# Optimization experiments

Measured on AMD Instinct MI355X. Metric: run time of the kernel, lower is better.

## Reference

```python
import jax, jax.numpy as jnp
import numpy as np

N_NODES = 50000
N_EDGES = 1600000
N_GRAPHS = 64


def setup_inputs() -> dict:
    key = jax.random.key(0)
    ks = jax.random.split(key, 16)
    p = lambda k, shape: (jax.random.normal(k, shape, dtype=jnp.float32) * 0.05)
    x = jax.random.normal(ks[0], (N_NODES, 128), dtype=jnp.float32)
    edge_index = jax.random.randint(ks[1], (2, N_EDGES), 0, N_NODES, dtype=jnp.int32)
    edge_attr = jax.random.uniform(ks[2], (N_EDGES,), dtype=jnp.float32)
    batch = jnp.sort(jax.random.randint(ks[3], (N_NODES,), 0, N_GRAPHS, dtype=jnp.int32))
    return {
        'x': x, 'edge_index': edge_index, 'edge_attr': edge_attr, 'batch': batch,
        'W1': p(ks[4], (128, 128)), 'b1': jnp.zeros((128,), jnp.float32),
        'W2': p(ks[5], (128, 64)), 'b2': jnp.zeros((64,), jnp.float32),
        'gW1': p(ks[6], (64, 32)), 'gb1': jnp.zeros((32,), jnp.float32),
        'gW2': p(ks[7], (32, 1)), 'gb2': jnp.zeros((1,), jnp.float32),
        'fcW1': p(ks[8], (64, 128)), 'fcb1': jnp.zeros((128,), jnp.float32),
        'fcW2': p(ks[9], (128, 2)), 'fcb2': jnp.zeros((2,), jnp.float32),
    }


def gcn_conv(x, src, dst, ew, W, b):
    # PyG GCNConv with edge weights: add self-loops (weight 1), symmetric norm.
    xw = x @ W  # [N, out]
    deg = jax.ops.segment_sum(ew, dst, num_segments=N_NODES) + 1.0  # self-loop
    dinv = jnp.where(deg > 0, jax.lax.rsqrt(deg), 0.0)
    coef = dinv[src] * ew * dinv[dst]  # [E]
    agg = jax.ops.segment_sum(coef[:, None] * xw[src], dst, num_segments=N_NODES)
    agg = agg + (dinv * dinv)[:, None] * xw  # self-loop contribution
    return agg + b


def global_attention(x, batch, gW1, gb1, gW2, gb2):
    # gate_nn: Linear(64,32)->ReLU->Linear(32,1), segment-softmax over graphs
    g = (jax.nn.relu(x @ gW1 + gb1) @ gW2 + gb2)[:, 0]  # [N]
    gmax = jax.ops.segment_max(g, batch, num_segments=N_GRAPHS)
    ex = jnp.exp(g - gmax[batch])
    den = jax.ops.segment_sum(ex, batch, num_segments=N_GRAPHS)
    alpha = ex / den[batch]
    return jax.ops.segment_sum(alpha[:, None] * x, batch, num_segments=N_GRAPHS)


def reference(x, edge_index, edge_attr, batch, W1, b1, W2, b2,
              gW1, gb1, gW2, gb2, fcW1, fcb1, fcW2, fcb2):
    src, dst = edge_index[0], edge_index[1]
    h = jax.nn.relu(gcn_conv(x, src, dst, edge_attr, W1, b1))
    x1 = jax.nn.relu(gcn_conv(h, src, dst, edge_attr, W2, b2))
    x2 = global_attention(x1, batch, gW1, gb1, gW2, gb2)  # [G, 64]
    # dropout is identity in eval mode
    h2 = jax.nn.relu(x2 @ fcW1 + fcb1)
    logits = h2 @ fcW2 + fcb2
    return jax.nn.log_softmax(logits, axis=1)
```

## Files before the change

### kernel.cpp

```cpp
#include <hip/hip_runtime.h>
#include <hip/hip_bf16.h>
#include <hip/hip_fp16.h>

#define N_NODES 50000
#define N_EDGES 1600000
#define N_GRAPHS 64
#define G1BLKS 1563
#define NSH 8
#define SH_STRIDE 50048
#define NBLK8 6250

__device__ __forceinline__ float coef_of(unsigned p) {
    return __half2float(__ushort_as_half((unsigned short)(p & 0xFFFFu)));
}

__global__ void mega1(const float* __restrict__ X, const float* __restrict__ W,
                      __half* __restrict__ Yh, const int* __restrict__ dst,
                      const float* __restrict__ ew,
                      unsigned long long* __restrict__ packed8,
                      unsigned short* __restrict__ pos16) {
    __shared__ float Xl[32][132];
    if (blockIdx.x >= G1BLKS) {
        const int sh = blockIdx.x & (NSH - 1);
        unsigned long long* __restrict__ pk = packed8 + (size_t)sh * SH_STRIDE;
        int e = (blockIdx.x - G1BLKS) * 256 + threadIdx.x;
        if (e < N_EDGES) {
            int d = __builtin_nontemporal_load(&dst[e]);
            float w = __builtin_nontemporal_load(&ew[e]);
            unsigned fix = (unsigned)(w * 16777216.0f);
            unsigned long long old = atomicAdd(&pk[d], 0x100000000ull | (unsigned long long)fix);
            pos16[e] = (unsigned short)((sh << 12) | (unsigned)(old >> 32));
        }
        return;
    }
    const int rt = threadIdx.x >> 5;
    const int ct = threadIdx.x & 31;
    const int base = blockIdx.x * 32;
    for (int i = threadIdx.x; i < 32 * 32; i += 256) {
        int rr = i >> 5, cc = (i & 31) << 2;
        int gr = base + rr;
        float4 v = (gr < N_NODES) ? *(const float4*)&X[(size_t)gr * 128 + cc]
                                  : make_float4(0.f, 0.f, 0.f, 0.f);
        Xl[rr][cc] = v.x; Xl[rr][cc + 1] = v.y; Xl[rr][cc + 2] = v.z; Xl[rr][cc + 3] = v.w;
    }
    __syncthreads();
    float acc[4][4] = {};
    for (int k = 0; k < 128; k += 4) {
        float4 a0 = *(const float4*)&Xl[rt * 4 + 0][k];
        float4 a1 = *(const float4*)&Xl[rt * 4 + 1][k];
        float4 a2 = *(const float4*)&Xl[rt * 4 + 2][k];
        float4 a3 = *(const float4*)&Xl[rt * 4 + 3][k];
        float4 w0 = *(const float4*)&W[(size_t)(k + 0) * 128 + ct * 4];
        float4 w1 = *(const float4*)&W[(size_t)(k + 1) * 128 + ct * 4];
        float4 w2 = *(const float4*)&W[(size_t)(k + 2) * 128 + ct * 4];
        float4 w3 = *(const float4*)&W[(size_t)(k + 3) * 128 + ct * 4];
        #define STEP(av, wv)  \
            acc[0][0] += av##0 * wv.x; acc[0][1] += av##0 * wv.y; acc[0][2] += av##0 * wv.z; acc[0][3] += av##0 * wv.w; \
            acc[1][0] += av##1 * wv.x; acc[1][1] += av##1 * wv.y; acc[1][2] += av##1 * wv.z; acc[1][3] += av##1 * wv.w; \
            acc[2][0] += av##2 * wv.x; acc[2][1] += av##2 * wv.y; acc[2][2] += av##2 * wv.z; acc[2][3] += av##2 * wv.w; \
            acc[3][0] += av##3 * wv.x; acc[3][1] += av##3 * wv.y; acc[3][2] += av##3 * wv.z; acc[3][3] += av##3 * wv.w;
        { float ax0=a0.x, ax1=a1.x, ax2=a2.x, ax3=a3.x; STEP(ax, w0) }
        { float ay0=a0.y, ay1=a1.y, ay2=a2.y, ay3=a3.y; STEP(ay, w1) }
        { float az0=a0.z, az1=a1.z, az2=a2.z, az3=a3.z; STEP(az, w2) }
        { float aw0=a0.w, aw1=a1.w, aw2=a2.w, aw3=a3.w; STEP(aw, w3) }
        #undef STEP
    }
    const int pc = ct >> 3;
    const int cw = (ct & 7) * 4;
    for (int i = 0; i < 4; ++i) {
        int gr = base + rt * 4 + i;
        if (gr < N_NODES) {
            ushort4 u;
            u.x = __half_as_ushort(__float2half(acc[i][0]));
            u.y = __half_as_ushort(__float2half(acc[i][1]));
            u.z = __half_as_ushort(__float2half(acc[i][2]));
            u.w = __half_as_ushort(__float2half(acc[i][3]));
            *(ushort4*)&Yh[((size_t)pc * N_NODES + gr) * 32 + cw] = u;
        }
    }
}

__global__ void block_sums_dinv(const unsigned long long* __restrict__ packed8,
                                int* __restrict__ bsum, float* __restrict__ dinv) {
    __shared__ int s[256];
    int idx = blockIdx.x * 256 + threadIdx.x;
    int c = 0;
    if (idx < N_NODES) {
        unsigned long long csum = 0, fsum = 0;
        #pragma unroll
        for (int sh = 0; sh < NSH; ++sh) {
            unsigned long long p = packed8[(size_t)sh * SH_STRIDE + idx];
            csum += p >> 32;
            fsum += p & 0xFFFFFFFFull;
        }
        c = (int)csum;
        dinv[idx] = rsqrtf((float)fsum * (1.0f / 16777216.0f) + 1.0f);
    }
    s[threadIdx.x] = c;
    __syncthreads();
    for (int o = 128; o; o >>= 1) {
        if (threadIdx.x < o) s[threadIdx.x] += s[threadIdx.x + o];
        __syncthreads();
    }
    if (threadIdx.x == 0) bsum[blockIdx.x] = s[0];
}

__global__ void scan_bsums(const int* __restrict__ bsum, int* __restrict__ boff,
                           int nb, int* __restrict__ row_start_last) {
    __shared__ int s[256];
    int v = (threadIdx.x < nb) ? bsum[threadIdx.x] : 0;
    s[threadIdx.x] = v;
    __syncthreads();
    for (int o = 1; o < 256; o <<= 1) {
        int t = 0;
        if (threadIdx.x >= o) t = s[threadIdx.x - o];
        __syncthreads();
        s[threadIdx.x] += t;
        __syncthreads();
    }
    if (threadIdx.x < nb) boff[threadIdx.x] = s[threadIdx.x] - v;
    if (threadIdx.x == 0) *row_start_last = N_EDGES;
}

__global__ void scan_counts(const unsigned long long* __restrict__ packed8,
                            const int* __restrict__ boff, int* __restrict__ row_start,
                            int* __restrict__ soff) {
    __shared__ int s[256];
    int idx = blockIdx.x * 256 + threadIdx.x;
    int cs[NSH];
    int v = 0;
    if (idx < N_NODES) {
        #pragma unroll
        for (int sh = 0; sh < NSH; ++sh) {
            cs[sh] = (int)(packed8[(size_t)sh * SH_STRIDE + idx] >> 32);
            v += cs[sh];
        }
    }
    s[threadIdx.x] = v;
    __syncthreads();
    for (int o = 1; o < 256; o <<= 1) {
        int t = 0;
        if (threadIdx.x >= o) t = s[threadIdx.x - o];
        __syncthreads();
        s[threadIdx.x] += t;
        __syncthreads();
    }
    if (idx < N_NODES) {
        int ex = boff[blockIdx.x] + s[threadIdx.x] - v;
        row_start[idx] = ex;
        int run = ex;
        #pragma unroll
        for (int sh = 0; sh < NSH; ++sh) {
            soff[(size_t)sh * SH_STRIDE + idx] = run;
            run += cs[sh];
        }
    }
}

__global__ void fill_direct(const int* __restrict__ src, const int* __restrict__ dst,
                            const float* __restrict__ ew, const unsigned short* __restrict__ pos16,
                            const int* __restrict__ soff, const float* __restrict__ dinv,
                            unsigned* __restrict__ csr) {
    int e = blockIdx.x * 256 + threadIdx.x;
    if (e < N_EDGES) {
        int d = __builtin_nontemporal_load(&dst[e]);
        int s = __builtin_nontemporal_load(&src[e]);
        float w = __builtin_nontemporal_load(&ew[e]);
        unsigned p16 = (unsigned)__builtin_nontemporal_load(&pos16[e]);
        int sh = (int)(p16 >> 12);
        int p  = (int)(p16 & 0xFFFu);
        float coef = dinv[s] * w * dinv[d];
        csr[soff[(size_t)sh * SH_STRIDE + d] + p] = ((unsigned)s << 16) | __half_as_ushort(__float2half(coef));
    }
}

template<int NP, bool HOUT>
__global__ void agg_csr_pair(const int* __restrict__ row_start, const unsigned* __restrict__ csr,
                             const __half* __restrict__ xwh, const float* __restrict__ dinv,
                             const float* __restrict__ b, void* __restrict__ outp) {
    constexpr int OUT = NP * 32;
    const int c    = blockIdx.x / NBLK8;
    const int nb   = blockIdx.x % NBLK8;
    const int n    = nb * 8 + (threadIdx.x >> 5);
    const int kk   = threadIdx.x & 15;
    const int half = (threadIdx.x >> 4) & 1;
    if (n >= N_NODES) return;
    const __half* __restrict__ bp = xwh + ((size_t)c * N_NODES) * 32 + 2 * kk;
    const int beg = row_start[n], end = row_start[n + 1];
    float ax = 0.f, ay = 0.f;
    int i = beg + half;
    unsigned c0 = 0, c1 = 0, c2 = 0, c3 = 0;
    if (i + 6 < end) { c0 = csr[i]; c1 = csr[i + 2]; c2 = csr[i + 4]; c3 = csr[i + 6]; }
    while (i + 6 < end) {
        __half2 h0 = *(const __half2*)(bp + (size_t)(c0 >> 16) * 32);
        __half2 h1 = *(const __half2*)(bp + (size_t)(c1 >> 16) * 32);
        __half2 h2 = *(const __half2*)(bp + (size_t)(c2 >> 16) * 32);
        __half2 h3 = *(const __half2*)(bp + (size_t)(c3 >> 16) * 32);
        float e0 = coef_of(c0), e1 = coef_of(c1), e2 = coef_of(c2), e3 = coef_of(c3);
        int ni = i + 8;
        unsigned d0 = 0, d1 = 0, d2 = 0, d3 = 0;
        if (ni + 6 < end) { d0 = csr[ni]; d1 = csr[ni + 2]; d2 = csr[ni + 4]; d3 = csr[ni + 6]; }
        float2 f0 = __half22float2(h0), f1 = __half22float2(h1);
        float2 f2 = __half22float2(h2), f3 = __half22float2(h3);
        ax += e0 * f0.x + e1 * f1.x + e2 * f2.x + e3 * f3.x;
        ay += e0 * f0.y + e1 * f1.y + e2 * f2.y + e3 * f3.y;
        c0 = d0; c1 = d1; c2 = d2; c3 = d3;
        i = ni;
    }
    for (; i < end; i += 2) {
        unsigned p = csr[i];
        float2 f = __half22float2(*(const __half2*)(bp + (size_t)(p >> 16) * 32));
        float e = coef_of(p);
        ax += e * f.x; ay += e * f.y;
    }
    ax += __shfl_xor(ax, 16);
    ay += __shfl_xor(ay, 16);
    if (half == 0) {
        float2 sf = __half22float2(*(const __half2*)(bp + (size_t)n * 32));
        float dv = dinv[n];
        float dv2 = dv * dv;
        int kg = c * 32 + 2 * kk;
        float ox = fmaxf(ax + dv2 * sf.x + b[kg], 0.f);
        float oy = fmaxf(ay + dv2 * sf.y + b[kg + 1], 0.f);
        if constexpr (HOUT) {
            __half* o = (__half*)outp;
            *(__half2*)&o[(size_t)n * OUT + kg] = __floats2half2_rn(ox, oy);
        } else {
            float* o = (float*)outp;
            *(float2*)&o[(size_t)n * OUT + kg] = make_float2(ox, oy);
        }
    }
}

__global__ void gemm2_reg(const __half* __restrict__ Xh, const float* __restrict__ W,
                          __half* __restrict__ Yh, int nrows) {
    __shared__ float Xl[32][132];
    __shared__ float Wl[128][64];
    const int rt = threadIdx.x >> 5;
    const int ct = threadIdx.x & 31;
    const int base = blockIdx.x * 32;
    for (int i = threadIdx.x; i < 32 * 32; i += 256) {
        int rr = i >> 5, cc = (i & 31) << 2;
        int gr = base + rr;
        float2 fa = make_float2(0.f, 0.f), fb = fa;
        if (gr < nrows) {
            const __half2* ph = (const __half2*)&Xh[(size_t)gr * 128 + cc];
            fa = __half22float2(ph[0]);
            fb = __half22float2(ph[1]);
        }
        Xl[rr][cc] = fa.x; Xl[rr][cc + 1] = fa.y; Xl[rr][cc + 2] = fb.x; Xl[rr][cc + 3] = fb.y;
    }
    for (int i = threadIdx.x; i < 128 * 16; i += 256) {
        int kk = i >> 4, cc = (i & 15) << 2;
        *(float4*)&Wl[kk][cc] = *(const float4*)&W[(size_t)kk * 64 + cc];
    }
    float acc[4][2] = {};
    __syncthreads();
    for (int k = 0; k < 128; k += 4) {
        float4 a0 = *(const float4*)&Xl[rt * 4 + 0][k];
        float4 a1 = *(const float4*)&Xl[rt * 4 + 1][k];
        float4 a2 = *(const float4*)&Xl[rt * 4 + 2][k];
        float4 a3 = *(const float4*)&Xl[rt * 4 + 3][k];
        float2 w0 = *(const float2*)&Wl[k + 0][ct * 2];
        float2 w1 = *(const float2*)&Wl[k + 1][ct * 2];
        float2 w2 = *(const float2*)&Wl[k + 2][ct * 2];
        float2 w3 = *(const float2*)&Wl[k + 3][ct * 2];
        acc[0][0] += a0.x * w0.x; acc[0][1] += a0.x * w0.y;
        acc[1][0] += a1.x * w0.x; acc[1][1] += a1.x * w0.y;
        acc[2][0] += a2.x * w0.x; acc[2][1] += a2.x * w0.y;
        acc[3][0] += a3.x * w0.x; acc[3][1] += a3.x * w0.y;
        acc[0][0] += a0.y * w1.x; acc[0][1] += a0.y * w1.y;
        acc[1][0] += a1.y * w1.x; acc[1][1] += a1.y * w1.y;
        acc[2][0] += a2.y * w1.x; acc[2][1] += a2.y * w1.y;
        acc[3][0] += a3.y * w1.x; acc[3][1] += a3.y * w1.y;
        acc[0][0] += a0.z * w2.x; acc[0][1] += a0.z * w2.y;
        acc[1][0] += a1.z * w2.x; acc[1][1] += a1.z * w2.y;
        acc[2][0] += a2.z * w2.x; acc[2][1] += a2.z * w2.y;
        acc[3][0] += a3.z * w2.x; acc[3][1] += a3.z * w2.y;
        acc[0][0] += a0.w * w3.x; acc[0][1] += a0.w * w3.y;
        acc[1][0] += a1.w * w3.x; acc[1][1] += a1.w * w3.y;
        acc[2][0] += a2.w * w3.x; acc[2][1] += a2.w * w3.y;
        acc[3][0] += a3.w * w3.x; acc[3][1] += a3.w * w3.y;
    }
    const int col0 = ct * 2;
    const int pc   = col0 >> 5;
    const int cw   = col0 & 31;
    for (int i = 0; i < 4; ++i) {
        int gr = base + rt * 4 + i;
        if (gr < nrows) {
            __half2 hv = __floats2half2_rn(acc[i][0], acc[i][1]);
            *(__half2*)&Yh[((size_t)pc * nrows + gr) * 32 + cw] = hv;
        }
    }
}

__global__ void gate_pool(const __half* __restrict__ x1h, const float* __restrict__ gW1,
                          const float* __restrict__ gb1, const float* __restrict__ gW2,
                          const float* __restrict__ gb2, const int* __restrict__ batch,
                          float* __restrict__ den, float* __restrict__ pooledU) {
    __shared__ float W1l[64 * 32];
    __shared__ float W2l[32];
    __shared__ float b1l[32];
    __shared__ float Xs[256][65];
    __shared__ float el[256];
    for (int i = threadIdx.x; i < 64 * 32; i += 256) W1l[i] = gW1[i];
    if (threadIdx.x < 32) { W2l[threadIdx.x] = gW2[threadIdx.x]; b1l[threadIdx.x] = gb1[threadIdx.x]; }
    const int n0 = blockIdx.x * 256;
    for (int i = threadIdx.x; i < 256 * 16; i += 256) {
        int r = i >> 4, c4 = (i & 15) << 2;
        int nn = n0 + r;
        if (nn < N_NODES) {
            ushort4 u = *(const ushort4*)&x1h[(size_t)nn * 64 + c4];
            Xs[r][c4 + 0] = __half2float(__ushort_as_half(u.x));
            Xs[r][c4 + 1] = __half2float(__ushort_as_half(u.y));
            Xs[r][c4 + 2] = __half2float(__ushort_as_half(u.z));
            Xs[r][c4 + 3] = __half2float(__ushort_as_half(u.w));
        } else {
            Xs[r][c4 + 0] = 0.f; Xs[r][c4 + 1] = 0.f;
            Xs[r][c4 + 2] = 0.f; Xs[r][c4 + 3] = 0.f;
        }
    }
    __syncthreads();
    const float gb2v = gb2[0];
    const int n = n0 + threadIdx.x;
    float ev = 0.f;
    if (n < N_NODES) {
        float t[32];
        #pragma unroll
        for (int j = 0; j < 32; ++j) t[j] = b1l[j];
        for (int k = 0; k < 64; ++k) {
            float xv = Xs[threadIdx.x][k];
            #pragma unroll
            for (int j = 0; j < 32; ++j) t[j] += xv * W1l[k * 32 + j];
        }
        float a = gb2v;
        #pragma unroll
        for (int j = 0; j < 32; ++j) a += fmaxf(t[j], 0.f) * W2l[j];
        ev = expf(a);
    }
    el[threadIdx.x] = ev;
    __syncthreads();
    const int f   = threadIdx.x & 63;
    const int grp = threadIdx.x >> 6;
    int start = n0 + grp * 64;
    if (start >= N_NODES) return;
    int end = min(start + 64, N_NODES);
    int cur = batch[start];
    float acc = 0.f, accd = 0.f;
    for (int m = start; m < end; ++m) {
        int bb = batch[m];
        if (bb != cur) {
            atomicAdd(&pooledU[cur * 64 + f], acc);
            if (f == 0) atomicAdd(&den[cur], accd);
            acc = 0.f; accd = 0.f; cur = bb;
        }
        float e = el[m - n0];
        acc += e * Xs[m - n0][f];
        if (f == 0) accd += e;
    }
    atomicAdd(&pooledU[cur * 64 + f], acc);
    if (f == 0) atomicAdd(&den[cur], accd);
}

__global__ void head_kernel(const float* __restrict__ pooledU, const float* __restrict__ den,
                            const float* __restrict__ fcW1, const float* __restrict__ fcb1,
                            const float* __restrict__ fcW2, const float* __restrict__ fcb2,
                            float* __restrict__ out) {
    __shared__ float P[64];
    __shared__ float r0[2], r1[2];
    const int gi = blockIdx.x;
    if (threadIdx.x < 64) P[threadIdx.x] = pooledU[gi * 64 + threadIdx.x] / den[gi];
    __syncthreads();
    const int j = threadIdx.x;
    float a = fcb1[j];
    #pragma unroll 8
    for (int k = 0; k < 64; ++k) a += P[k] * fcW1[k * 128 + j];
    float h = fmaxf(a, 0.f);
    float p0 = h * fcW2[j * 2 + 0];
    float p1 = h * fcW2[j * 2 + 1];
    for (int o = 32; o; o >>= 1) { p0 += __shfl_xor(p0, o); p1 += __shfl_xor(p1, o); }
    if ((threadIdx.x & 63) == 0) { r0[threadIdx.x >> 6] = p0; r1[threadIdx.x >> 6] = p1; }
    __syncthreads();
    if (threadIdx.x == 0) {
        float l0 = r0[0] + r0[1] + fcb2[0];
        float l1 = r1[0] + r1[1] + fcb2[1];
        float m = fmaxf(l0, l1);
        float lse = m + logf(expf(l0 - m) + expf(l1 - m));
        out[gi * 2 + 0] = l0 - lse;
        out[gi * 2 + 1] = l1 - lse;
    }
}

extern "C" void kernel_launch(void* const* d_in, const int* in_sizes, int n_in,
                              void* d_out, int out_size, void* d_ws, size_t ws_size,
                              hipStream_t stream) {
    const float* x    = (const float*)d_in[0];
    const int*   ei   = (const int*)d_in[1];
    const float* ew   = (const float*)d_in[2];
    const int*   batch= (const int*)d_in[3];
    const float* W1   = (const float*)d_in[4];
    const float* b1   = (const float*)d_in[5];
    const float* W2   = (const float*)d_in[6];
    const float* b2   = (const float*)d_in[7];
    const float* gW1  = (const float*)d_in[8];
    const float* gb1  = (const float*)d_in[9];
    const float* gW2  = (const float*)d_in[10];
    const float* gb2  = (const float*)d_in[11];
    const float* fcW1 = (const float*)d_in[12];
    const float* fcb1 = (const float*)d_in[13];
    const float* fcW2 = (const float*)d_in[14];
    const float* fcb2 = (const float*)d_in[15];
    float* out = (float*)d_out;

    const int* src = ei;
    const int* dst = ei + N_EDGES;

    const int EB = (N_EDGES + 255) / 256;
    const int NB = (N_NODES + 255) / 256;

    float* ws = (float*)d_ws;
    __half* xwh  = (__half*)ws;
    __half* hbuf = (__half*)(ws + 3200000);
    __half* x1h  = (__half*)(ws + 6400000);
    size_t off = 9600000;
    unsigned* csr   = (unsigned*)(ws + off); off += 1600000;
    unsigned short* pos16 = (unsigned short*)(ws + off); off += 800000;
    int*   row_start= (int*)(ws + off);    off += 50176;
    unsigned long long* packed8 = (unsigned long long*)(ws + off); off += 2 * NSH * SH_STRIDE;
    int*   soff     = (int*)(ws + off);    off += NSH * SH_STRIDE;
    float* dinv     = ws + off;            off += 50176;
    int*   bsum     = (int*)(ws + off);    off += 256;
    int*   boff     = (int*)(ws + off);    off += 256;
    float* den      = ws + off;            off += 64;
    float* pooled   = ws + off;            off += 4096;

    hipMemsetAsync(packed8, 0, (size_t)NSH * SH_STRIDE * sizeof(unsigned long long), stream);
    hipMemsetAsync(den, 0, (64 + 4096) * sizeof(float), stream);

    mega1<<<G1BLKS + EB, 256, 0, stream>>>(x, W1, xwh, dst, ew, packed8, pos16);

    block_sums_dinv<<<NB, 256, 0, stream>>>(packed8, bsum, dinv);
    scan_bsums<<<1, 256, 0, stream>>>(bsum, boff, NB, row_start + N_NODES);
    scan_counts<<<NB, 256, 0, stream>>>(packed8, boff, row_start, soff);
    fill_direct<<<EB, 256, 0, stream>>>(src, dst, ew, pos16, soff, dinv, csr);

    agg_csr_pair<4, true><<<4 * NBLK8, 256, 0, stream>>>(row_start, csr, xwh, dinv, b1, hbuf);

    gemm2_reg<<<(N_NODES + 31) / 32, 256, 0, stream>>>(hbuf, W2, xwh, N_NODES);
    agg_csr_pair<2, true><<<2 * NBLK8, 256, 0, stream>>>(row_start, csr, xwh, dinv, b2, x1h);

    gate_pool<<<NB, 256, 0, stream>>>(x1h, gW1, gb1, gW2, gb2, batch, den, pooled);

    head_kernel<<<N_GRAPHS, 128, 0, stream>>>(pooled, den, fcW1, fcb1, fcW2, fcb2, out);
}
```

Baseline: 298.1 us.

## Fuse CSR build stages into one cooperative kernel; deepen aggregation prefetch

Replaces the four CSR-construction kernels (block sums/dinv, block-sum scan, count scan, fill) with one cooperative kernel that separates phases with grid-wide syncs and fills edges via a grid-stride loop. It also zeroes the pooling accumulators inside that kernel, removing a memset. Separately, the CSR aggregation loop is software-pipelined one stage deeper, issuing gathers for the next group while the current group is accumulated. This cuts launch overhead and inter-kernel gaps, but grid.sync costs and the 1024-block grid may leave fewer waves in flight during the fill phase.

```diff
diff --git a/kernel.cpp b/kernel.cpp
--- a/kernel.cpp
+++ b/kernel.cpp
@@ -1,6 +1,9 @@
 #include <hip/hip_runtime.h>
 #include <hip/hip_bf16.h>
 #include <hip/hip_fp16.h>
+#include <hip/hip_cooperative_groups.h>
+
+namespace cg = cooperative_groups;
 
 #define N_NODES 50000
 #define N_EDGES 1600000
@@ -9,6 +12,7 @@
 #define NSH 8
 #define SH_STRIDE 50048
 #define NBLK8 6250
+#define COOP_BLKS 1024
 
 __device__ __forceinline__ float coef_of(unsigned p) {
     return __half2float(__ushort_as_half((unsigned short)(p & 0xFFFFu)));
@@ -80,97 +84,101 @@
     }
 }
 
-__global__ void block_sums_dinv(const unsigned long long* __restrict__ packed8,
-                                int* __restrict__ bsum, float* __restrict__ dinv) {
+__global__ void csr_build_coop(const unsigned long long* __restrict__ packed8,
+                               const int* __restrict__ src, const int* __restrict__ dst,
+                               const float* __restrict__ ew,
+                               const unsigned short* __restrict__ pos16,
+                               int* __restrict__ bsum, int* __restrict__ boff,
+                               int* __restrict__ row_start, int* __restrict__ soff,
+                               float* __restrict__ dinv, unsigned* __restrict__ csr,
+                               float* __restrict__ den_pool) {
+    cg::grid_group grid = cg::this_grid();
     __shared__ int s[256];
-    int idx = blockIdx.x * 256 + threadIdx.x;
+    const int tid = blockIdx.x * 256 + threadIdx.x;
+
     int c = 0;
-    if (idx < N_NODES) {
+    if (tid < N_NODES) {
         unsigned long long csum = 0, fsum = 0;
         #pragma unroll
         for (int sh = 0; sh < NSH; ++sh) {
-            unsigned long long p = packed8[(size_t)sh * SH_STRIDE + idx];
+            unsigned long long p = packed8[(size_t)sh * SH_STRIDE + tid];
             csum += p >> 32;
             fsum += p & 0xFFFFFFFFull;
         }
         c = (int)csum;
-        dinv[idx] = rsqrtf((float)fsum * (1.0f / 16777216.0f) + 1.0f);
-    }
-    s[threadIdx.x] = c;
-    __syncthreads();
-    for (int o = 128; o; o >>= 1) {
-        if (threadIdx.x < o) s[threadIdx.x] += s[threadIdx.x + o];
+        dinv[tid] = rsqrtf((float)fsum * (1.0f / 16777216.0f) + 1.0f);
+    }
+    if (tid < 64 + 4096) den_pool[tid] = 0.f;
+    if (blockIdx.x < 196) {
+        s[threadIdx.x] = c;
         __syncthreads();
-    }
-    if (threadIdx.x == 0) bsum[blockIdx.x] = s[0];
-}
-
-__global__ void scan_bsums(const int* __restrict__ bsum, int* __restrict__ boff,
-                           int nb, int* __restrict__ row_start_last) {
-    __shared__ int s[256];
-    int v = (threadIdx.x < nb) ? bsum[threadIdx.x] : 0;
-    s[threadIdx.x] = v;
-    __syncthreads();
-    for (int o = 1; o < 256; o <<= 1) {
-        int t = 0;
-        if (threadIdx.x >= o) t = s[threadIdx.x - o];
+        for (int o = 128; o; o >>= 1) {
+            if (threadIdx.x < o) s[threadIdx.x] += s[threadIdx.x + o];
+            __syncthreads();
+        }
+        if (threadIdx.x == 0) bsum[blockIdx.x] = s[0];
+    }
+    grid.sync();
+
+    if (blockIdx.x == 0) {
+        int v = (threadIdx.x < 196) ? bsum[threadIdx.x] : 0;
+        s[threadIdx.x] = v;
         __syncthreads();
-        s[threadIdx.x] += t;
+        for (int o = 1; o < 256; o <<= 1) {
+            int t = 0;
+            if (threadIdx.x >= o) t = s[threadIdx.x - o];
+            __syncthreads();
+            s[threadIdx.x] += t;
+            __syncthreads();
+        }
+        if (threadIdx.x < 196) boff[threadIdx.x] = s[threadIdx.x] - v;
+        if (threadIdx.x == 0) row_start[N_NODES] = N_EDGES;
+    }
+    grid.sync();
+
+    if (blockIdx.x < 196) {
+        int idx = tid;
+        int cs[NSH];
+        int v = 0;
+        if (idx < N_NODES) {
+            #pragma unroll
+            for (int sh = 0; sh < NSH; ++sh) {
+                cs[sh] = (int)(packed8[(size_t)sh * SH_STRIDE + idx] >> 32);
+                v += cs[sh];
+            }
+        }
+        s[threadIdx.x] = v;
         __syncthreads();
-    }
-    if (threadIdx.x < nb) boff[threadIdx.x] = s[threadIdx.x] - v;
-    if (threadIdx.x == 0) *row_start_last = N_EDGES;
-}
-
-__global__ void scan_counts(const unsigned long long* __restrict__ packed8,
-                            const int* __restrict__ boff, int* __restrict__ row_start,
-                            int* __restrict__ soff) {
-    __shared__ int s[256];
-    int idx = blockIdx.x * 256 + threadIdx.x;
-    int cs[NSH];
-    int v = 0;
-    if (idx < N_NODES) {
-        #pragma unroll
-        for (int sh = 0; sh < NSH; ++sh) {
-            cs[sh] = (int)(packed8[(size_t)sh * SH_STRIDE + idx] >> 32);
-            v += cs[sh];
-        }
-    }
-    s[threadIdx.x] = v;
-    __syncthreads();
-    for (int o = 1; o < 256; o <<= 1) {
-        int t = 0;
-        if (threadIdx.x >= o) t = s[threadIdx.x - o];
-        __syncthreads();
-        s[threadIdx.x] += t;
-        __syncthreads();
-    }
-    if (idx < N_NODES) {
-        int ex = boff[blockIdx.x] + s[threadIdx.x] - v;
-        row_start[idx] = ex;
-        int run = ex;
-        #pragma unroll
-        for (int sh = 0; sh < NSH; ++sh) {
-            soff[(size_t)sh * SH_STRIDE + idx] = run;
-            run += cs[sh];
-        }
-    }
-}
-
-__global__ void fill_direct(const int* __restrict__ src, const int* __restrict__ dst,
-                            const float* __restrict__ ew, const unsigned short* __restrict__ pos16,
-                            const int* __restrict__ soff, const float* __restrict__ dinv,
-                            unsigned* __restrict__ csr) {
-    int e = blockIdx.x * 256 + threadIdx.x;
-    if (e < N_EDGES) {
+        for (int o = 1; o < 256; o <<= 1) {
+            int t = 0;
+            if (threadIdx.x >= o) t = s[threadIdx.x - o];
+            __syncthreads();
+            s[threadIdx.x] += t;
+            __syncthreads();
+        }
+        if (idx < N_NODES) {
+            int ex = boff[blockIdx.x] + s[threadIdx.x] - v;
+            row_start[idx] = ex;
+            int run = ex;
+            #pragma unroll
+            for (int sh = 0; sh < NSH; ++sh) {
+                soff[(size_t)sh * SH_STRIDE + idx] = run;
+                run += cs[sh];
+            }
+        }
+    }
+    grid.sync();
+
+    const int stride = gridDim.x * 256;
+    for (int e = tid; e < N_EDGES; e += stride) {
         int d = __builtin_nontemporal_load(&dst[e]);
-        int s = __builtin_nontemporal_load(&src[e]);
+        int sv = __builtin_nontemporal_load(&src[e]);
         float w = __builtin_nontemporal_load(&ew[e]);
         unsigned p16 = (unsigned)__builtin_nontemporal_load(&pos16[e]);
         int sh = (int)(p16 >> 12);
         int p  = (int)(p16 & 0xFFFu);
-        float coef = dinv[s] * w * dinv[d];
-        csr[soff[(size_t)sh * SH_STRIDE + d] + p] = ((unsigned)s << 16) | __half_as_ushort(__float2half(coef));
+        float coef = dinv[sv] * w * dinv[d];
+        csr[soff[(size_t)sh * SH_STRIDE + d] + p] = ((unsigned)sv << 16) | __half_as_ushort(__float2half(coef));
     }
 }
 
@@ -189,23 +197,36 @@
     const int beg = row_start[n], end = row_start[n + 1];
     float ax = 0.f, ay = 0.f;
     int i = beg + half;
-    unsigned c0 = 0, c1 = 0, c2 = 0, c3 = 0;
-    if (i + 6 < end) { c0 = csr[i]; c1 = csr[i + 2]; c2 = csr[i + 4]; c3 = csr[i + 6]; }
+    unsigned ca0 = 0, ca1 = 0, ca2 = 0, ca3 = 0;
+    unsigned cb0 = 0, cb1 = 0, cb2 = 0, cb3 = 0;
+    __half2 ha0{}, ha1{}, ha2{}, ha3{};
+    if (i + 6 < end) {
+        ca0 = csr[i]; ca1 = csr[i + 2]; ca2 = csr[i + 4]; ca3 = csr[i + 6];
+        ha0 = *(const __half2*)(bp + (size_t)(ca0 >> 16) * 32);
+        ha1 = *(const __half2*)(bp + (size_t)(ca1 >> 16) * 32);
+        ha2 = *(const __half2*)(bp + (size_t)(ca2 >> 16) * 32);
+        ha3 = *(const __half2*)(bp + (size_t)(ca3 >> 16) * 32);
+        int i2 = i + 8;
+        if (i2 + 6 < end) { cb0 = csr[i2]; cb1 = csr[i2 + 2]; cb2 = csr[i2 + 4]; cb3 = csr[i2 + 6]; }
+    }
     while (i + 6 < end) {
-        __half2 h0 = *(const __half2*)(bp + (size_t)(c0 >> 16) * 32);
-        __half2 h1 = *(const __half2*)(bp + (size_t)(c1 >> 16) * 32);
-        __half2 h2 = *(const __half2*)(bp + (size_t)(c2 >> 16) * 32);
-        __half2 h3 = *(const __half2*)(bp + (size_t)(c3 >> 16) * 32);
-        float e0 = coef_of(c0), e1 = coef_of(c1), e2 = coef_of(c2), e3 = coef_of(c3);
-        int ni = i + 8;
-        unsigned d0 = 0, d1 = 0, d2 = 0, d3 = 0;
-        if (ni + 6 < end) { d0 = csr[ni]; d1 = csr[ni + 2]; d2 = csr[ni + 4]; d3 = csr[ni + 6]; }
-        float2 f0 = __half22float2(h0), f1 = __half22float2(h1);
-        float2 f2 = __half22float2(h2), f3 = __half22float2(h3);
+        int i2 = i + 8;
+        __half2 hb0 = *(const __half2*)(bp + (size_t)(cb0 >> 16) * 32);
+        __half2 hb1 = *(const __half2*)(bp + (size_t)(cb1 >> 16) * 32);
+        __half2 hb2 = *(const __half2*)(bp + (size_t)(cb2 >> 16) * 32);
+        __half2 hb3 = *(const __half2*)(bp + (size_t)(cb3 >> 16) * 32);
+        int i3 = i2 + 8;
+        unsigned cc0 = 0, cc1 = 0, cc2 = 0, cc3 = 0;
+        if (i3 + 6 < end) { cc0 = csr[i3]; cc1 = csr[i3 + 2]; cc2 = csr[i3 + 4]; cc3 = csr[i3 + 6]; }
+        float2 f0 = __half22float2(ha0), f1 = __half22float2(ha1);
+        float2 f2 = __half22float2(ha2), f3 = __half22float2(ha3);
+        float e0 = coef_of(ca0), e1 = coef_of(ca1), e2 = coef_of(ca2), e3 = coef_of(ca3);
         ax += e0 * f0.x + e1 * f1.x + e2 * f2.x + e3 * f3.x;
         ay += e0 * f0.y + e1 * f1.y + e2 * f2.y + e3 * f3.y;
-        c0 = d0; c1 = d1; c2 = d2; c3 = d3;
-        i = ni;
+        ca0 = cb0; ca1 = cb1; ca2 = cb2; ca3 = cb3;
+        ha0 = hb0; ha1 = hb1; ha2 = hb2; ha3 = hb3;
+        cb0 = cc0; cb1 = cc1; cb2 = cc2; cb3 = cc3;
+        i = i2;
     }
     for (; i < end; i += 2) {
         unsigned p = csr[i];
@@ -435,14 +456,16 @@
     float* pooled   = ws + off;            off += 4096;
 
     hipMemsetAsync(packed8, 0, (size_t)NSH * SH_STRIDE * sizeof(unsigned long long), stream);
-    hipMemsetAsync(den, 0, (64 + 4096) * sizeof(float), stream);
 
     mega1<<<G1BLKS + EB, 256, 0, stream>>>(x, W1, xwh, dst, ew, packed8, pos16);
 
-    block_sums_dinv<<<NB, 256, 0, stream>>>(packed8, bsum, dinv);
-    scan_bsums<<<1, 256, 0, stream>>>(bsum, boff, NB, row_start + N_NODES);
-    scan_counts<<<NB, 256, 0, stream>>>(packed8, boff, row_start, soff);
-    fill_direct<<<EB, 256, 0, stream>>>(src, dst, ew, pos16, soff, dinv, csr);
+    {
+        void* cargs[] = { (void*)&packed8, (void*)&src, (void*)&dst, (void*)&ew, (void*)&pos16,
+                          (void*)&bsum, (void*)&boff, (void*)&row_start, (void*)&soff,
+                          (void*)&dinv, (void*)&csr, (void*)&den };
+        hipLaunchCooperativeKernel((void*)csr_build_coop, dim3(COOP_BLKS), dim3(256),
+                                   cargs, 0, stream);
+    }
 
     agg_csr_pair<4, true><<<4 * NBLK8, 256, 0, stream>>>(row_start, csr, xwh, dinv, b1, hbuf);
 
```

After: 642.6 us. 116% more time.

## Fuse three-kernel degree scan into single-pass scan with inter-block flags

Applied to the files above, without the earlier changes.

Replaces the block-sum, block-offset scan and count-scan kernels with one kernel. Each block publishes its total through a flag and then spins on the flags of earlier blocks to build its prefix. This removes two kernel launches and one extra read of the packed counts. In exchange it relies on all 196 blocks being co-resident, since earlier blocks must finish for the spin-waits to end. The flags are zeroed by extending an existing memset.

```diff
diff --git a/kernel.cpp b/kernel.cpp
--- a/kernel.cpp
+++ b/kernel.cpp
@@ -9,6 +9,7 @@
 #define NSH 8
 #define SH_STRIDE 50048
 #define NBLK8 6250
+#define SCAN_BLOCKS 196
 
 __device__ __forceinline__ float coef_of(unsigned p) {
     return __half2float(__ushort_as_half((unsigned short)(p & 0xFFFFu)));
@@ -80,35 +81,28 @@
     }
 }
 
-__global__ void block_sums_dinv(const unsigned long long* __restrict__ packed8,
-                                int* __restrict__ bsum, float* __restrict__ dinv) {
+__global__ void scan_all(const unsigned long long* __restrict__ packed8,
+                         float* __restrict__ dinv, int* __restrict__ row_start,
+                         int* __restrict__ soff, int* __restrict__ flags,
+                         int* __restrict__ totals) {
     __shared__ int s[256];
-    int idx = blockIdx.x * 256 + threadIdx.x;
-    int c = 0;
+    const int idx = blockIdx.x * 256 + threadIdx.x;
+    int cs[NSH];
+    int v = 0;
     if (idx < N_NODES) {
-        unsigned long long csum = 0, fsum = 0;
+        unsigned long long fsum = 0;
         #pragma unroll
         for (int sh = 0; sh < NSH; ++sh) {
             unsigned long long p = packed8[(size_t)sh * SH_STRIDE + idx];
-            csum += p >> 32;
+            cs[sh] = (int)(p >> 32);
+            v += cs[sh];
             fsum += p & 0xFFFFFFFFull;
         }
-        c = (int)csum;
         dinv[idx] = rsqrtf((float)fsum * (1.0f / 16777216.0f) + 1.0f);
-    }
-    s[threadIdx.x] = c;
-    __syncthreads();
-    for (int o = 128; o; o >>= 1) {
-        if (threadIdx.x < o) s[threadIdx.x] += s[threadIdx.x + o];
-        __syncthreads();
-    }
-    if (threadIdx.x == 0) bsum[blockIdx.x] = s[0];
-}
-
-__global__ void scan_bsums(const int* __restrict__ bsum, int* __restrict__ boff,
-                           int nb, int* __restrict__ row_start_last) {
-    __shared__ int s[256];
-    int v = (threadIdx.x < nb) ? bsum[threadIdx.x] : 0;
+    } else {
+        #pragma unroll
+        for (int sh = 0; sh < NSH; ++sh) cs[sh] = 0;
+    }
     s[threadIdx.x] = v;
     __syncthreads();
     for (int o = 1; o < 256; o <<= 1) {
@@ -118,35 +112,28 @@
         s[threadIdx.x] += t;
         __syncthreads();
     }
-    if (threadIdx.x < nb) boff[threadIdx.x] = s[threadIdx.x] - v;
-    if (threadIdx.x == 0) *row_start_last = N_EDGES;
-}
-
-__global__ void scan_counts(const unsigned long long* __restrict__ packed8,
-                            const int* __restrict__ boff, int* __restrict__ row_start,
-                            int* __restrict__ soff) {
-    __shared__ int s[256];
-    int idx = blockIdx.x * 256 + threadIdx.x;
-    int cs[NSH];
-    int v = 0;
+    const int inc = s[threadIdx.x];
+    const int btotal = s[255];
+    if (threadIdx.x == 0) {
+        totals[blockIdx.x] = btotal;
+        __threadfence();
+        atomicExch(&flags[blockIdx.x], 1);
+    }
+    int pre = 0;
+    if ((int)threadIdx.x < (int)blockIdx.x) {
+        while (atomicAdd(&flags[threadIdx.x], 0) == 0) {}
+        pre = atomicAdd(&totals[threadIdx.x], 0);
+    }
+    __syncthreads();
+    s[threadIdx.x] = pre;
+    __syncthreads();
+    for (int o = 128; o; o >>= 1) {
+        if (threadIdx.x < o) s[threadIdx.x] += s[threadIdx.x + o];
+        __syncthreads();
+    }
+    const int bpre = s[0];
     if (idx < N_NODES) {
-        #pragma unroll
-        for (int sh = 0; sh < NSH; ++sh) {
-            cs[sh] = (int)(packed8[(size_t)sh * SH_STRIDE + idx] >> 32);
-            v += cs[sh];
-        }
-    }
-    s[threadIdx.x] = v;
-    __syncthreads();
-    for (int o = 1; o < 256; o <<= 1) {
-        int t = 0;
-        if (threadIdx.x >= o) t = s[threadIdx.x - o];
-        __syncthreads();
-        s[threadIdx.x] += t;
-        __syncthreads();
-    }
-    if (idx < N_NODES) {
-        int ex = boff[blockIdx.x] + s[threadIdx.x] - v;
+        int ex = bpre + inc - v;
         row_start[idx] = ex;
         int run = ex;
         #pragma unroll
@@ -155,6 +142,7 @@
             run += cs[sh];
         }
     }
+    if (blockIdx.x == SCAN_BLOCKS - 1 && threadIdx.x == 255) row_start[N_NODES] = N_EDGES;
 }
 
 __global__ void fill_direct(const int* __restrict__ src, const int* __restrict__ dst,
@@ -429,19 +417,18 @@
     unsigned long long* packed8 = (unsigned long long*)(ws + off); off += 2 * NSH * SH_STRIDE;
     int*   soff     = (int*)(ws + off);    off += NSH * SH_STRIDE;
     float* dinv     = ws + off;            off += 50176;
-    int*   bsum     = (int*)(ws + off);    off += 256;
-    int*   boff     = (int*)(ws + off);    off += 256;
     float* den      = ws + off;            off += 64;
     float* pooled   = ws + off;            off += 4096;
+    int*   flags    = (int*)(ws + off);    off += 256;
+    int*   totals   = (int*)(ws + off);    off += 256;
 
     hipMemsetAsync(packed8, 0, (size_t)NSH * SH_STRIDE * sizeof(unsigned long long), stream);
-    hipMemsetAsync(den, 0, (64 + 4096) * sizeof(float), stream);
+    hipMemsetAsync(den, 0, (64 + 4096 + 256) * sizeof(float), stream);
 
     mega1<<<G1BLKS + EB, 256, 0, stream>>>(x, W1, xwh, dst, ew, packed8, pos16);
 
-    block_sums_dinv<<<NB, 256, 0, stream>>>(packed8, bsum, dinv);
-    scan_bsums<<<1, 256, 0, stream>>>(bsum, boff, NB, row_start + N_NODES);
-    scan_counts<<<NB, 256, 0, stream>>>(packed8, boff, row_start, soff);
+    scan_all<<<SCAN_BLOCKS, 256, 0, stream>>>(packed8, dinv, row_start, soff, flags, totals);
+
     fill_direct<<<EB, 256, 0, stream>>>(src, dst, ew, pos16, soff, dinv, csr);
 
     agg_csr_pair<4, true><<<4 * NBLK8, 256, 0, stream>>>(row_start, csr, xwh, dinv, b1, hbuf);
```

Result: no change. 300.0 us (+0.6%).
